# Kernel tuning notes

Measured on AMD Instinct MI355X. Metric: run time of the kernel, lower is better.

Reference implementation:

```python
import jax, jax.numpy as jnp
import numpy as np

B, T, I, H, O = 32, 2048, 12, 512, 3
L = 3  # GRU layers


def _gru_layer(x_seq, h0, w_ih, w_hh, b_ih, b_hh):
    # x_seq: [B,T,D], h0: [B,H]; PyTorch gate order: r, z, n
    xW = jnp.einsum('btd,gd->btg', x_seq, w_ih) + b_ih  # [B,T,3H]

    def step(h, xw_t):
        hw = h @ w_hh.T + b_hh                  # [B,3H]
        xr, xz, xn = jnp.split(xw_t, 3, axis=-1)
        hr, hz, hn = jnp.split(hw, 3, axis=-1)
        r = jax.nn.sigmoid(xr + hr)
        z = jax.nn.sigmoid(xz + hz)
        n = jnp.tanh(xn + r * hn)
        h_new = (1.0 - z) * n + z * h
        return h_new, h_new

    h_last, ys = jax.lax.scan(step, h0, jnp.swapaxes(xW, 0, 1))  # ys: [T,B,H]
    return jnp.swapaxes(ys, 0, 1), h_last


def _prelu(x, a):
    return jnp.where(x >= 0, x, a * x)


def setup_inputs() -> dict:
    key = jax.random.key(0)
    ks = jax.random.split(key, 40)
    s = 1.0 / np.sqrt(H)

    def u(k, shape):
        return jax.random.uniform(k, shape, jnp.float32, -s, s)

    inp = {
        'x': jax.random.normal(ks[0], (B, T, I), jnp.float32),
        'vel_init': jax.random.normal(ks[1], (B, 1, 3), jnp.float32),
    }
    in_dims = [I, H, H]
    for l in range(L):
        inp[f'w_ih_{l}'] = u(ks[2 + 4 * l], (3 * H, in_dims[l]))
        inp[f'w_hh_{l}'] = u(ks[3 + 4 * l], (3 * H, H))
        inp[f'b_ih_{l}'] = u(ks[4 + 4 * l], (3 * H,))
        inp[f'b_hh_{l}'] = u(ks[5 + 4 * l], (3 * H,))
    inp['a1'] = jnp.array([0.25], jnp.float32)  # PReLU (single shared param)
    inp['dec_in_w'] = u(ks[14], (H, I)); inp['dec_in_b'] = u(ks[15], (H,))
    inp['vd0_w'] = u(ks[16], (H, 3)); inp['vd0_b'] = u(ks[17], (H,))
    inp['vd1_w'] = u(ks[18], (H, 3)); inp['vd1_b'] = u(ks[19], (H,))
    inp['vd2_w'] = u(ks[20], (H, 3)); inp['vd2_b'] = u(ks[21], (H,))
    inp['vel_w'] = u(ks[22], (O, H)); inp['vel_b'] = u(ks[23], (O,))
    inp['std_w'] = u(ks[24], (O, H)); inp['std_b'] = u(ks[25], (O,))
    inp['attn_w'] = u(ks[26], (1, H)); inp['attn_b'] = u(ks[27], (1,))
    return inp


def reference(x, vel_init, w_ih_0, w_hh_0, b_ih_0, b_hh_0,
              w_ih_1, w_hh_1, b_ih_1, b_hh_1,
              w_ih_2, w_hh_2, b_ih_2, b_hh_2,
              a1, dec_in_w, dec_in_b,
              vd0_w, vd0_b, vd1_w, vd1_b, vd2_w, vd2_b,
              vel_w, vel_b, std_w, std_b, attn_w, attn_b):
    v0 = vel_init[:, 0, :]  # [B,3]
    # h0 per layer from velocity decoders (permute(1,0,2)+cat -> layer axis)
    h0s = [v0 @ vd0_w.T + vd0_b, v0 @ vd1_w.T + vd1_b, v0 @ vd2_w.T + vd2_b]
    w_ih = [w_ih_0, w_ih_1, w_ih_2]
    w_hh = [w_hh_0, w_hh_1, w_hh_2]
    b_ih = [b_ih_0, b_ih_1, b_ih_2]
    b_hh = [b_hh_0, b_hh_1, b_hh_2]

    out = x
    for l in range(L):
        out, _ = _gru_layer(out, h0s[l], w_ih[l], w_hh[l], b_ih[l], b_hh[l])

    out = _prelu(out, a1)
    # softmax skip-attention over time dim
    scores = jnp.einsum('bth,oh->bto', out, attn_w) + attn_b      # [B,T,1]
    attn = jax.nn.softmax(scores, axis=1)
    out = out + attn * (jnp.einsum('bti,hi->bth', x, dec_in_w) + dec_in_b)

    vel = jnp.einsum('bth,oh->bto', out, vel_w) + vel_b
    std = jnp.einsum('bth,oh->bto', out, std_w) + std_b
    return vel, std
```

## Files before the change

### kernel.cpp

```cpp
#include <hip/hip_runtime.h>
#include <stdint.h>


#define B_ 32
#define T_ 2048
#define H_ 512
#define R_ 128
#define HR_ 8

typedef __attribute__((ext_vector_type(8))) short s8v;
typedef __attribute__((ext_vector_type(4))) float f4v;
typedef __attribute__((ext_vector_type(4))) uint32_t u32x4;
typedef __attribute__((ext_vector_type(2))) unsigned short u16x2;

__device__ __forceinline__ uint16_t f2bf(float f){ return __builtin_bit_cast(uint16_t, (__bf16)f); }
__device__ __forceinline__ float bf2f(uint16_t b){ return __builtin_bit_cast(float, ((uint32_t)b)<<16); }

__device__ __forceinline__ s8v pack8(const float* f){
  s8v r;
  #pragma unroll
  for (int i=0;i<8;++i) r[i] = (short)f2bf(f[i]);
  return r;
}
__device__ __forceinline__ f4v mfma16(s8v a, s8v b, f4v c){
  return __builtin_amdgcn_mfma_f32_16x16x32_bf16(a,b,c,0,0,0);
}
#if __has_builtin(__builtin_amdgcn_rcpf)
__device__ __forceinline__ float rcp_(float x){ return __builtin_amdgcn_rcpf(x); }
#else
__device__ __forceinline__ float rcp_(float x){ return 1.0f/x; }
#endif
__device__ __forceinline__ float sigm(float s){ return rcp_(1.f + __expf(-s)); }
__device__ __forceinline__ float tanh2(float v){ return 1.f - 2.f*rcp_(1.f + __expf(2.f*v)); }

__device__ __forceinline__ u32x4 load_x4_sc(const void* p){
  u32x4 r;
  asm volatile("global_load_dwordx4 %0, %1, off sc0 sc1" : "=v"(r) : "v"(p) : "memory");
  return r;
}
__device__ __forceinline__ u32x4 load_x4_sc_wait(const void* p){
  u32x4 r;
  asm volatile("global_load_dwordx4 %0, %1, off sc0 sc1\n\ts_waitcnt vmcnt(0)"
               : "=v"(r) : "v"(p) : "memory");
  return r;
}
__device__ __forceinline__ uint32_t load_u32_sc_wait(const void* p){
  uint32_t r;
  asm volatile("global_load_dword %0, %1, off sc0 sc1\n\ts_waitcnt vmcnt(0)"
               : "=v"(r) : "v"(p) : "memory");
  return r;
}
__device__ __forceinline__ void store_s16_sc(void* p, uint32_t v){
  asm volatile("global_store_short %0, %1, off sc0 sc1" :: "v"(p), "v"(v) : "memory");
}
__device__ __forceinline__ void store_u32_sc(void* p, uint32_t v){
  asm volatile("global_store_dword %0, %1, off sc0 sc1" :: "v"(p), "v"(v) : "memory");
}
__device__ __forceinline__ u32x4 load_x4_l2(const void* p){
  u32x4 r;
  asm volatile("global_load_dwordx4 %0, %1, off sc0" : "=v"(r) : "v"(p) : "memory");
  return r;
}
__device__ __forceinline__ void store_s16_l2(void* p, uint32_t v){
  asm volatile("global_store_short %0, %1, off sc0" :: "v"(p), "v"(v) : "memory");
}

__device__ __forceinline__ void load16(u32x4* a, const uint16_t* base, bool l2){
  if (l2) {
    #pragma unroll
    for (int ks=0; ks<16; ++ks) a[ks] = load_x4_l2(base + ks*32);
  } else {
    #pragma unroll
    for (int ks=0; ks<16; ++ks) a[ks] = load_x4_sc(base + ks*32);
  }
}

__device__ __forceinline__ bool chunk_ok(u32x4 c){
  u16x2 m = __builtin_bit_cast(u16x2, c[0]);
  m = __builtin_elementwise_max(m, __builtin_bit_cast(u16x2, c[1]));
  m = __builtin_elementwise_max(m, __builtin_bit_cast(u16x2, c[2]));
  m = __builtin_elementwise_max(m, __builtin_bit_cast(u16x2, c[3]));
  unsigned short mm = (m[0] > m[1]) ? m[0] : m[1];
  return mm != (unsigned short)0xFFFFu;
}
__device__ __forceinline__ bool valid16(const u32x4* a){
  u16x2 m = {0, 0};
  #pragma unroll
  for (int c=0;c<16;++c){
    #pragma unroll
    for (int i=0;i<4;++i)
      m = __builtin_elementwise_max(m, __builtin_bit_cast(u16x2, a[c][i]));
  }
  unsigned short mm = (m[0] > m[1]) ? m[0] : m[1];
  return mm != (unsigned short)0xFFFFu;
}

__device__ __forceinline__ uint32_t get_xcc(){
  uint32_t x;
  asm volatile("s_getreg_b32 %0, hwreg(HW_REG_XCC_ID)" : "=s"(x));
  return x & 7u;
}
__device__ __forceinline__ uint64_t realtime_(){
  uint64_t t;
  asm volatile("s_memrealtime %0\n\ts_waitcnt lgkmcnt(0)" : "=s"(t));
  return t;
}

__global__ void poison_kernel(uint32_t* p, unsigned int n16)
{
  u32x4 v = {0xFFFFFFFFu, 0xFFFFFFFFu, 0xFFFFFFFFu, 0xFFFFFFFFu};
  for (unsigned int k = blockIdx.x*blockDim.x + threadIdx.x; k < n16;
       k += gridDim.x*blockDim.x)
    ((u32x4*)p)[k] = v;
}

__global__ void init_kernel(const float* __restrict__ vel_init,
    const float* __restrict__ w0, const float* __restrict__ b0,
    const float* __restrict__ w1, const float* __restrict__ b1,
    const float* __restrict__ w2, const float* __restrict__ b2,
    float* __restrict__ h0f, uint16_t* __restrict__ h0b,
    uint32_t* progress, uint32_t* claimp)
{
  const int l = blockIdx.x, tid = threadIdx.x;
  const float* w  = (l==0)?w0:((l==1)?w1:w2);
  const float* bb = (l==0)?b0:((l==1)?b1:b2);
  for (int idx = tid; idx < B_*H_; idx += 256){
    int b = idx >> 9, j = idx & 511;
    float s = bb[j] + vel_init[b*3+0]*w[j*3+0] + vel_init[b*3+1]*w[j*3+1]
                    + vel_init[b*3+2]*w[j*3+2];
    h0f[(size_t)l*(B_*H_) + idx] = s;
    h0b[(size_t)l*(B_*H_) + idx] = f2bf(s);
  }
  if (l == 0 && tid < 192) progress[tid] = 0;
  if (l == 0 && tid >= 192 && tid < 200) claimp[tid-192] = 0;
}

struct ScanParams {
  const float* x;
  const float* wih[3];
  const float* whh[3];
  const float* bih[3];
  const float* bhh[3];
  const float* h0f;
  const uint16_t* h0b;
  uint16_t* xr0;
  uint16_t* xr1;
  uint16_t* hr0;
  uint16_t* hr1;
  uint16_t* out2;
  uint32_t* progress;
  uint32_t* claimp;
};

__global__ __launch_bounds__(128, 1) void fused_scan(ScanParams P)
{
  const int tid  = threadIdx.x;
  const int lane = tid & 63;
  const int mt   = tid >> 6;
  const int u    = lane & 15;
  const int lq   = lane >> 4;
  const int ko   = lq * 8;
  const int bd   = lq * 4;

  __shared__ uint16_t lds[48*512];
  __shared__ char pad_[36864];
  __shared__ int sh_role[3];
  if (P.x == nullptr) ((volatile char*)pad_)[0] = 1;

  if (tid == 0){
    int layer = -1, wg = -1, home = 0;
    uint32_t xcc = get_xcc();
    if (xcc < 3u){
      unsigned s = atomicAdd(&P.claimp[xcc], 1u);
      if (s < 32u){ layer = (int)xcc; wg = (int)s; home = 1; }
    }
    if (layer < 0){
      uint64_t t0 = realtime_();
      while (realtime_() - t0 < 5000ull) __builtin_amdgcn_s_sleep(32);
      for (;;){
        bool allfull = true;
        for (int l=0; l<3 && layer<0; ++l){
          if (__hip_atomic_load(&P.claimp[l], __ATOMIC_RELAXED,
                                __HIP_MEMORY_SCOPE_AGENT) < 32u){
            allfull = false;
            unsigned s = atomicAdd(&P.claimp[l], 1u);
            if (s < 32u){ layer = l; wg = (int)s; home = (xcc == (uint32_t)l); }
          }
        }
        if (layer >= 0 || allfull) break;
        __builtin_amdgcn_s_sleep(16);
      }
    }
    int fast = 0;
    if (layer >= 0){
      if (!home) atomicAdd(&P.claimp[4], 1u);
      __hip_atomic_fetch_add(&P.claimp[3], 1u, __ATOMIC_ACQ_REL,
                             __HIP_MEMORY_SCOPE_AGENT);
      while (__hip_atomic_load(&P.claimp[3], __ATOMIC_ACQUIRE,
                               __HIP_MEMORY_SCOPE_AGENT) < 96u)
        __builtin_amdgcn_s_sleep(8);
      fast = (__hip_atomic_load(&P.claimp[4], __ATOMIC_ACQUIRE,
                                __HIP_MEMORY_SCOPE_AGENT) == 0u) ? 1 : 0;
    }
    sh_role[0] = layer; sh_role[1] = wg; sh_role[2] = fast;
  }
  __syncthreads();
  const int layer = sh_role[0];
  if (layer < 0) return;
  const int wg = sh_role[1];
  const bool fastmode = (sh_role[2] != 0);
  const int j0 = wg * 16;

  const float* wih = P.wih[layer];
  const float* whh = P.whh[layer];
  const float* bih = P.bih[layer];
  const float* bhh = P.bhh[layer];

  const float bs0 = bih[0*H_ + j0 + u] + bhh[0*H_ + j0 + u];
  const float bs1 = bih[1*H_ + j0 + u] + bhh[1*H_ + j0 + u];
  const float bi2 = bih[2*H_ + j0 + u];
  const float bh2 = bhh[2*H_ + j0 + u];

  s8v whhf[3][16];
  #pragma unroll
  for (int nt=0; nt<3; ++nt){
    #pragma unroll
    for (int ks=0; ks<16; ++ks){
      const float* wp = whh + (size_t)(nt*H_ + j0 + u)*H_ + ks*32 + ko;
      float tmp[8];
      #pragma unroll
      for (int i=0;i<8;++i) tmp[i] = wp[i];
      whhf[nt][ks] = pack8(tmp);
    }
  }

  s8v w0f[3];
  if (layer == 0){
    #pragma unroll
    for (int nt=0; nt<3; ++nt){
      float tmp[8];
      #pragma unroll
      for (int i=0;i<8;++i){
        int k = ko + i;
        tmp[i] = (k < 12) ? wih[(size_t)(nt*H_ + j0 + u)*12 + k] : 0.f;
      }
      w0f[nt] = pack8(tmp);
    }
  } else {
    for (int e = tid; e < (48*512)/8; e += 128) {
      int idx = e * 8;
      int g = idx >> 9, k = idx & 511;
      const float* wp = wih + (size_t)((g>>4)*H_ + j0 + (g&15))*H_ + k;
      float tmp[8];
      #pragma unroll
      for (int i=0;i<8;++i) tmp[i] = wp[i];
      s8v v = pack8(tmp);
      uint32_t msk = (uint32_t)((((g&7) ^ (((g>>3)&1)<<1))) << 4);
      uint32_t off = (uint32_t)g*1024u + ((((uint32_t)k)*2u) ^ msk);
      *(u32x4*)((char*)lds + off) = __builtin_bit_cast(u32x4, v);
    }
  }
  __syncthreads();

  const uint16_t* inring = (layer==1) ? P.xr0 : P.xr1;
  uint16_t* hring = (layer==0) ? P.hr0 : P.hr1;
  uint16_t* xout  = (layer==0) ? P.xr0 : P.xr1;
  uint32_t* myprog = P.progress + layer*64 + wg*2 + mt;
  const uint32_t* nextprog = (layer<2) ? (P.progress + (layer+1)*64) : nullptr;

  float hold[4];
  #pragma unroll
  for (int r=0;r<4;++r)
    hold[r] = P.h0f[(size_t)layer*(B_*H_) + (size_t)(mt*16 + bd + r)*H_ + j0 + u];

  const uint32_t sw  = (uint32_t)((((u&7) ^ (((u>>3)&1)<<1))) << 4);
  const uint32_t gb0 = (uint32_t)((0*16 + u) * 1024);
  const uint32_t gb1 = (uint32_t)((1*16 + u) * 1024);
  const uint32_t gb2 = (uint32_t)((2*16 + u) * 1024);
  const uint32_t koB = (uint32_t)(ko * 2);
  const int cl = lane & 31;
  const size_t rowoff = (size_t)(mt*16 + bd)*H_ + j0 + u;

  bool hfast = fastmode;
  int poison_until = 63;

  u32x4 xa[16];
  auto issue_x = [&](int tt){
    const uint16_t* xin = inring + (size_t)(tt & (R_-1))*(B_*H_)
                          + (size_t)(mt*16+u)*H_ + ko;
    #pragma unroll
    for (int ks=0; ks<16; ++ks) xa[ks] = load_x4_sc(xin + ks*32);
  };
  if (layer > 0) issue_x(0);

  for (int t = 0; t < T_; ++t) {
    f4v ac0 = {0,0,0,0}, ac1 = {0,0,0,0}, axn = {0,0,0,0}, ahn = {0,0,0,0};

    if (layer > 0) {
      asm volatile("s_waitcnt vmcnt(0)" ::: "memory");
      __builtin_amdgcn_sched_barrier(0);
      if (__ballot(valid16(xa)) != ~0ull) {
        const uint16_t* xslot = inring + (size_t)(t & (R_-1))*(B_*H_);
        const uint16_t* xcan  = xslot + (size_t)(mt*16)*H_ + cl*16;
        do {
          while (1) {
            u32x4 c = load_x4_sc_wait(xcan);
            if (__ballot(chunk_ok(c)) == ~0ull) break;
            __builtin_amdgcn_s_sleep(2);
          }
          issue_x(t);
          asm volatile("s_waitcnt vmcnt(0)" ::: "memory");
          __builtin_amdgcn_sched_barrier(0);
        } while (__ballot(valid16(xa)) != ~0ull);
      }
    }

    const uint16_t* hsrc = (t == 0)
        ? (P.h0b + (size_t)layer*(B_*H_))
        : (layer == 2 ? (P.out2 + (size_t)(t-1)*(B_*H_))
                      : (hring + (size_t)((t-1) & (HR_-1))*(B_*H_)));
    const uint16_t* hp = hsrc + (size_t)(mt*16+u)*H_ + ko;
    u32x4 ha[16];
    load16(ha, hp, hfast);

    if (layer == 0) {
      const float* xp = P.x + ((size_t)(mt*16 + u)*T_ + (size_t)t)*12;
      float4 lo  = *(const float4*)(xp);
      float4 md  = *(const float4*)(xp + 4);
      float4 hi4 = *(const float4*)(xp + 8);
      float xv[8];
      xv[0] = (ko==0) ? lo.x : hi4.x;  xv[1] = (ko==0) ? lo.y : hi4.y;
      xv[2] = (ko==0) ? lo.z : hi4.z;  xv[3] = (ko==0) ? lo.w : hi4.w;
      xv[4] = (ko==0) ? md.x : 0.f;    xv[5] = (ko==0) ? md.y : 0.f;
      xv[6] = (ko==0) ? md.z : 0.f;    xv[7] = (ko==0) ? md.w : 0.f;
      s8v a = pack8(xv);
      ac0 = mfma16(a, w0f[0], ac0);
      ac1 = mfma16(a, w0f[1], ac1);
      axn = mfma16(a, w0f[2], axn);
    } else {
      #pragma unroll
      for (int ks=0; ks<16; ++ks){
        s8v a = __builtin_bit_cast(s8v, xa[ks]);
        uint32_t kk = ((uint32_t)(ks*64) + koB) ^ sw;
        s8v w0 = *(const s8v*)((const char*)lds + gb0 + kk);
        s8v w1 = *(const s8v*)((const char*)lds + gb1 + kk);
        s8v w2 = *(const s8v*)((const char*)lds + gb2 + kk);
        ac0 = mfma16(a, w0, ac0);
        ac1 = mfma16(a, w1, ac1);
        axn = mfma16(a, w2, axn);
      }
    }

    asm volatile("s_waitcnt vmcnt(0)" ::: "memory");
    __builtin_amdgcn_sched_barrier(0);
    if (t > 0) {
      int spins = 0;
      while (__ballot(valid16(ha)) != ~0ull) {
        if (++spins > 512) hfast = false;
        __builtin_amdgcn_s_sleep(1);
        load16(ha, hp, hfast);
        asm volatile("s_waitcnt vmcnt(0)" ::: "memory");
        __builtin_amdgcn_sched_barrier(0);
      }
    }

    #pragma unroll
    for (int ks=0; ks<16; ++ks){
      s8v a = __builtin_bit_cast(s8v, ha[ks]);
      ac0 = mfma16(a, whhf[0][ks], ac0);
      ac1 = mfma16(a, whhf[1][ks], ac1);
      ahn = mfma16(a, whhf[2][ks], ahn);
    }

    if (layer < 2) {
      uint16_t* hrow = hring + (size_t)(t & (HR_-1))*(B_*H_) + rowoff;
      uint16_t* xrow = xout  + (size_t)(t & (R_-1))*(B_*H_) + rowoff;
      #pragma unroll
      for (int r=0;r<4;++r){
        float rg = sigm(ac0[r] + bs0);
        float zg = sigm(ac1[r] + bs1);
        float ng = tanh2(axn[r] + bi2 + rg*(ahn[r] + bh2));
        float hv = ng + zg*(hold[r] - ng);
        hold[r] = hv;
        uint32_t bv = (uint32_t)f2bf(hv);
        if (fastmode) store_s16_l2(hrow + (size_t)r*H_, bv);
        else          store_s16_sc(hrow + (size_t)r*H_, bv);
        store_s16_sc(xrow + (size_t)r*H_, bv);
      }
      uint16_t* prow = hring + (size_t)((t+4) & (HR_-1))*(B_*H_) + rowoff;
      #pragma unroll
      for (int r=0;r<4;++r){
        if (fastmode) store_s16_l2(prow + (size_t)r*H_, 0xFFFFu);
        else          store_s16_sc(prow + (size_t)r*H_, 0xFFFFu);
      }
    } else {
      uint16_t* orow = P.out2 + (size_t)t*(B_*H_) + rowoff;
      #pragma unroll
      for (int r=0;r<4;++r){
        float rg = sigm(ac0[r] + bs0);
        float zg = sigm(ac1[r] + bs1);
        float ng = tanh2(axn[r] + bi2 + rg*(ahn[r] + bh2));
        float hv = ng + zg*(hold[r] - ng);
        hold[r] = hv;
        uint32_t bv = (uint32_t)f2bf(hv);
        if (fastmode) store_s16_l2(orow + (size_t)r*H_, bv);
        else          store_s16_sc(orow + (size_t)r*H_, bv);
      }
    }

    if (layer > 0 && (t & 15) == 15 && lane == 0)
      store_u32_sc(myprog, (uint32_t)t);

    if (layer < 2 && t >= 64) {
      if (t > poison_until) {
        while (1) {
          int c = (int)load_u32_sc_wait(nextprog + lane);
          #pragma unroll
          for (int off=32; off>0; off>>=1){
            int c2 = __shfl_xor(c, off, 64);
            c = (c2 < c) ? c2 : c;
          }
          poison_until = c + 60;
          if (t <= poison_until) break;
          __builtin_amdgcn_s_sleep(8);
        }
      }
      uint16_t* qrow = xout + (size_t)((t+64) & (R_-1))*(B_*H_) + rowoff;
      #pragma unroll
      for (int r=0;r<4;++r) store_s16_sc(qrow + (size_t)r*H_, 0xFFFFu);
    }

    if (layer > 0 && t+1 < T_) issue_x(t+1);
  }
}

__global__ void scores_kernel(const uint16_t* __restrict__ out2,
    const float* __restrict__ attn_w, const float* __restrict__ attn_b,
    const float* __restrict__ a1, float* __restrict__ scores)
{
  int gw = (blockIdx.x * blockDim.x + threadIdx.x) >> 6;
  int lane = threadIdx.x & 63;
  int b = gw >> 11, t = gw & 2047;
  float alpha = a1[0];
  u32x4 q = *(const u32x4*)(out2 + ((size_t)t*B_ + b)*H_ + lane*8);
  const uint16_t* ob = (const uint16_t*)&q;
  const float* aw = attn_w + lane*8;
  float acc = 0.f;
  #pragma unroll
  for (int i=0;i<8;++i){
    float ov = bf2f(ob[i]);
    ov = (ov >= 0.f) ? ov : alpha*ov;
    acc += ov * aw[i];
  }
  #pragma unroll
  for (int off=32; off>0; off>>=1) acc += __shfl_xor(acc, off, 64);
  if (lane == 0) scores[(size_t)b*T_ + t] = acc + attn_b[0];
}

__global__ void softmax_kernel(const float* __restrict__ scores, float* __restrict__ attn)
{
  int b = blockIdx.x, tid = threadIdx.x;
  __shared__ float red[256];
  const float* row = scores + (size_t)b*T_;
  float v[8]; float m = -3.4e38f;
  #pragma unroll
  for (int i=0;i<8;++i){ v[i] = row[tid + i*256]; m = fmaxf(m, v[i]); }
  red[tid] = m; __syncthreads();
  for (int s=128; s>0; s>>=1){ if (tid < s) red[tid] = fmaxf(red[tid], red[tid+s]); __syncthreads(); }
  m = red[0]; __syncthreads();
  float sum = 0.f;
  #pragma unroll
  for (int i=0;i<8;++i){ v[i] = __expf(v[i]-m); sum += v[i]; }
  red[tid] = sum; __syncthreads();
  for (int s=128; s>0; s>>=1){ if (tid < s) red[tid] += red[tid+s]; __syncthreads(); }
  float inv = 1.f / red[0];
  #pragma unroll
  for (int i=0;i<8;++i) attn[(size_t)b*T_ + tid + i*256] = v[i]*inv;
}

__global__ void final_kernel(const uint16_t* __restrict__ out2, const float* __restrict__ x,
    const float* __restrict__ attn, const float* __restrict__ dw, const float* __restrict__ db,
    const float* __restrict__ vw, const float* __restrict__ vb,
    const float* __restrict__ swt, const float* __restrict__ sb,
    const float* __restrict__ a1, float* __restrict__ dout)
{
  int gw = (blockIdx.x * blockDim.x + threadIdx.x) >> 6;
  int lane = threadIdx.x & 63;
  int b = gw >> 11, t = gw & 2047;
  float alpha = a1[0];
  u32x4 q = *(const u32x4*)(out2 + ((size_t)t*B_ + b)*H_ + lane*8);
  const uint16_t* ob = (const uint16_t*)&q;
  const float* xp = x + ((size_t)b*T_ + t)*12;
  float xr[12];
  #pragma unroll
  for (int i=0;i<12;++i) xr[i] = xp[i];
  float av = attn[(size_t)b*T_ + t];
  float acc[6] = {0,0,0,0,0,0};
  #pragma unroll
  for (int k=0;k<8;++k){
    int j = lane*8 + k;
    float ov = bf2f(ob[k]);
    ov = (ov >= 0.f) ? ov : alpha*ov;
    float d = db[j];
    const float* dwp = dw + (size_t)j*12;
    #pragma unroll
    for (int i=0;i<12;++i) d += xr[i]*dwp[i];
    float uo = ov + av*d;
    #pragma unroll
    for (int o=0;o<3;++o){
      acc[o]   += uo * vw[(size_t)o*H_ + j];
      acc[3+o] += uo * swt[(size_t)o*H_ + j];
    }
  }
  #pragma unroll
  for (int o=0;o<6;++o){
    #pragma unroll
    for (int off=32; off>0; off>>=1) acc[o] += __shfl_xor(acc[o], off, 64);
  }
  if (lane == 0){
    size_t p = ((size_t)b*T_ + t)*3;
    #pragma unroll
    for (int o=0;o<3;++o){
      dout[p + o] = acc[o] + vb[o];
      dout[(size_t)B_*T_*3 + p + o] = acc[3+o] + sb[o];
    }
  }
}

extern "C" void kernel_launch(void* const* d_in, const int* in_sizes, int n_in,
                              void* d_out, int out_size, void* d_ws, size_t ws_size,
                              hipStream_t stream)
{
  (void)in_sizes; (void)n_in; (void)out_size; (void)ws_size;
  const float* x        = (const float*)d_in[0];
  const float* vel_init = (const float*)d_in[1];
  const float* w_ih[3] = {(const float*)d_in[2], (const float*)d_in[6],  (const float*)d_in[10]};
  const float* w_hh[3] = {(const float*)d_in[3], (const float*)d_in[7],  (const float*)d_in[11]};
  const float* b_ih[3] = {(const float*)d_in[4], (const float*)d_in[8],  (const float*)d_in[12]};
  const float* b_hh[3] = {(const float*)d_in[5], (const float*)d_in[9],  (const float*)d_in[13]};
  const float* a1     = (const float*)d_in[14];
  const float* dec_w  = (const float*)d_in[15];
  const float* dec_b  = (const float*)d_in[16];
  const float* vd_w[3] = {(const float*)d_in[17], (const float*)d_in[19], (const float*)d_in[21]};
  const float* vd_b[3] = {(const float*)d_in[18], (const float*)d_in[20], (const float*)d_in[22]};
  const float* vel_w  = (const float*)d_in[23];
  const float* vel_b  = (const float*)d_in[24];
  const float* std_w  = (const float*)d_in[25];
  const float* std_b  = (const float*)d_in[26];
  const float* attn_w = (const float*)d_in[27];
  const float* attn_b = (const float*)d_in[28];

  char* ws = (char*)d_ws;
  uint16_t* out2   = (uint16_t*)(ws);
  uint16_t* xr0    = (uint16_t*)(ws + (size_t)67108864);
  uint16_t* xr1    = (uint16_t*)(ws + (size_t)71303168);
  uint16_t* hr0    = (uint16_t*)(ws + (size_t)75497472);
  uint16_t* hr1    = (uint16_t*)(ws + (size_t)75759616);
  float*    h0f    = (float*)   (ws + (size_t)76021760);
  uint16_t* h0b    = (uint16_t*)(ws + (size_t)76218368);
  float*    scores = (float*)   (ws + (size_t)76316672);
  float*    attnp  = (float*)   (ws + (size_t)76578816);
  uint32_t* progress = (uint32_t*)(ws + (size_t)76840960);
  uint32_t* claimp   = (uint32_t*)(ws + (size_t)76841728);

  poison_kernel<<<2048, 256, 0, stream>>>((uint32_t*)ws, 76021760u/16u);
  init_kernel<<<3, 256, 0, stream>>>(vel_init, vd_w[0], vd_b[0], vd_w[1], vd_b[1],
                                     vd_w[2], vd_b[2], h0f, h0b, progress, claimp);

  ScanParams P;
  P.x = x;
  for (int l=0;l<3;++l){ P.wih[l]=w_ih[l]; P.whh[l]=w_hh[l]; P.bih[l]=b_ih[l]; P.bhh[l]=b_hh[l]; }
  P.h0f = h0f; P.h0b = h0b;
  P.xr0 = xr0; P.xr1 = xr1; P.hr0 = hr0; P.hr1 = hr1;
  P.out2 = out2; P.progress = progress; P.claimp = claimp;

  fused_scan<<<256, 128, 0, stream>>>(P);

  scores_kernel<<<(B_*T_)/4, 256, 0, stream>>>(out2, attn_w, attn_b, a1, scores);
  softmax_kernel<<<B_, 256, 0, stream>>>(scores, attnp);
  final_kernel<<<(B_*T_)/4, 256, 0, stream>>>(out2, x, attnp, dec_w, dec_b,
                                              vel_w, vel_b, std_w, std_b, a1, (float*)d_out);
}
```

Baseline: 8.520 ms.

## Replace poison-based x ring handoff with progress-counter sync between GRU layers

Layers now synchronise on the inter-layer x ring through per-workgroup progress counters instead of poisoning slots and spinning on sentinel values. Layer 2 gets its own small recurrent h ring rather than reading back from the large output buffer. The poison kernel now clears only the h rings, not the whole 76MB workspace. This removes the large poison launch and the ring-poison stores, and it overlaps the h load with waiting on x, at the cost of polling the counters and a vmcnt drain every 16 steps.

```diff
diff --git a/kernel.cpp b/kernel.cpp
--- a/kernel.cpp
+++ b/kernel.cpp
@@ -38,12 +38,6 @@
   asm volatile("global_load_dwordx4 %0, %1, off sc0 sc1" : "=v"(r) : "v"(p) : "memory");
   return r;
 }
-__device__ __forceinline__ u32x4 load_x4_sc_wait(const void* p){
-  u32x4 r;
-  asm volatile("global_load_dwordx4 %0, %1, off sc0 sc1\n\ts_waitcnt vmcnt(0)"
-               : "=v"(r) : "v"(p) : "memory");
-  return r;
-}
 __device__ __forceinline__ uint32_t load_u32_sc_wait(const void* p){
   uint32_t r;
   asm volatile("global_load_dword %0, %1, off sc0 sc1\n\ts_waitcnt vmcnt(0)"
@@ -65,8 +59,8 @@
   asm volatile("global_store_short %0, %1, off sc0" :: "v"(p), "v"(v) : "memory");
 }
 
-__device__ __forceinline__ void load16(u32x4* a, const uint16_t* base, bool l2){
-  if (l2) {
+__device__ __forceinline__ void load16f(u32x4* a, const uint16_t* base, bool fast){
+  if (fast) {
     #pragma unroll
     for (int ks=0; ks<16; ++ks) a[ks] = load_x4_l2(base + ks*32);
   } else {
@@ -74,15 +68,10 @@
     for (int ks=0; ks<16; ++ks) a[ks] = load_x4_sc(base + ks*32);
   }
 }
-
-__device__ __forceinline__ bool chunk_ok(u32x4 c){
-  u16x2 m = __builtin_bit_cast(u16x2, c[0]);
-  m = __builtin_elementwise_max(m, __builtin_bit_cast(u16x2, c[1]));
-  m = __builtin_elementwise_max(m, __builtin_bit_cast(u16x2, c[2]));
-  m = __builtin_elementwise_max(m, __builtin_bit_cast(u16x2, c[3]));
-  unsigned short mm = (m[0] > m[1]) ? m[0] : m[1];
-  return mm != (unsigned short)0xFFFFu;
-}
+__device__ __forceinline__ void st16f(void* p, uint32_t v, bool fast){
+  if (fast) store_s16_l2(p, v); else store_s16_sc(p, v);
+}
+
 __device__ __forceinline__ bool valid16(const u32x4* a){
   u16x2 m = {0, 0};
   #pragma unroll
@@ -147,6 +136,7 @@
   uint16_t* xr1;
   uint16_t* hr0;
   uint16_t* hr1;
+  uint16_t* hr2;
   uint16_t* out2;
   uint32_t* progress;
   uint32_t* claimp;
@@ -263,9 +253,10 @@
   __syncthreads();
 
   const uint16_t* inring = (layer==1) ? P.xr0 : P.xr1;
-  uint16_t* hring = (layer==0) ? P.hr0 : P.hr1;
-  uint16_t* xout  = (layer==0) ? P.xr0 : P.xr1;
+  uint16_t* xout = (layer==0) ? P.xr0 : P.xr1;
+  uint16_t* hring = (layer==0) ? P.hr0 : ((layer==1) ? P.hr1 : P.hr2);
   uint32_t* myprog = P.progress + layer*64 + wg*2 + mt;
+  const uint32_t* prevprog = (layer>0) ? (P.progress + (layer-1)*64) : nullptr;
   const uint32_t* nextprog = (layer<2) ? (P.progress + (layer+1)*64) : nullptr;
 
   float hold[4];
@@ -282,7 +273,9 @@
   const size_t rowoff = (size_t)(mt*16 + bd)*H_ + j0 + u;
 
   bool hfast = fastmode;
-  int poison_until = 63;
+  int xprog = 0;
+  int consprog = 0;
+  bool xpref = false;
 
   u32x4 xa[16];
   auto issue_x = [&](int tt){
@@ -291,37 +284,36 @@
     #pragma unroll
     for (int ks=0; ks<16; ++ks) xa[ks] = load_x4_sc(xin + ks*32);
   };
-  if (layer > 0) issue_x(0);
+  auto poll32 = [&](const uint32_t* base)->int{
+    int c = (int)load_u32_sc_wait(base + 2*cl + mt);
+    #pragma unroll
+    for (int off=16; off>0; off>>=1){
+      int c2 = __shfl_xor(c, off, 64);
+      c = (c2 < c) ? c2 : c;
+    }
+    return c;
+  };
 
   for (int t = 0; t < T_; ++t) {
     f4v ac0 = {0,0,0,0}, ac1 = {0,0,0,0}, axn = {0,0,0,0}, ahn = {0,0,0,0};
 
-    if (layer > 0) {
-      asm volatile("s_waitcnt vmcnt(0)" ::: "memory");
-      __builtin_amdgcn_sched_barrier(0);
-      if (__ballot(valid16(xa)) != ~0ull) {
-        const uint16_t* xslot = inring + (size_t)(t & (R_-1))*(B_*H_);
-        const uint16_t* xcan  = xslot + (size_t)(mt*16)*H_ + cl*16;
-        do {
-          while (1) {
-            u32x4 c = load_x4_sc_wait(xcan);
-            if (__ballot(chunk_ok(c)) == ~0ull) break;
-            __builtin_amdgcn_s_sleep(2);
-          }
-          issue_x(t);
-          asm volatile("s_waitcnt vmcnt(0)" ::: "memory");
-          __builtin_amdgcn_sched_barrier(0);
-        } while (__ballot(valid16(xa)) != ~0ull);
+    const uint16_t* hslot = (t == 0)
+        ? (P.h0b + (size_t)layer*(B_*H_))
+        : (hring + (size_t)((t-1) & (HR_-1))*(B_*H_));
+    const uint16_t* hp = hslot + (size_t)(mt*16+u)*H_ + ko;
+    u32x4 ha[16];
+    load16f(ha, hp, hfast);
+
+    if (layer > 0 && !xpref) {
+      while (xprog < t+1) {
+        xprog = poll32(prevprog);
+        if (xprog < t+1) __builtin_amdgcn_s_sleep(4);
       }
-    }
-
-    const uint16_t* hsrc = (t == 0)
-        ? (P.h0b + (size_t)layer*(B_*H_))
-        : (layer == 2 ? (P.out2 + (size_t)(t-1)*(B_*H_))
-                      : (hring + (size_t)((t-1) & (HR_-1))*(B_*H_)));
-    const uint16_t* hp = hsrc + (size_t)(mt*16+u)*H_ + ko;
-    u32x4 ha[16];
-    load16(ha, hp, hfast);
+      issue_x(t);
+    }
+
+    asm volatile("s_waitcnt vmcnt(0)" ::: "memory");
+    __builtin_amdgcn_sched_barrier(0);
 
     if (layer == 0) {
       const float* xp = P.x + ((size_t)(mt*16 + u)*T_ + (size_t)t)*12;
@@ -351,14 +343,12 @@
       }
     }
 
-    asm volatile("s_waitcnt vmcnt(0)" ::: "memory");
-    __builtin_amdgcn_sched_barrier(0);
     if (t > 0) {
       int spins = 0;
       while (__ballot(valid16(ha)) != ~0ull) {
         if (++spins > 512) hfast = false;
         __builtin_amdgcn_s_sleep(1);
-        load16(ha, hp, hfast);
+        load16f(ha, hp, hfast);
         asm volatile("s_waitcnt vmcnt(0)" ::: "memory");
         __builtin_amdgcn_sched_barrier(0);
       }
@@ -372,65 +362,46 @@
       ahn = mfma16(a, whhf[2][ks], ahn);
     }
 
-    if (layer < 2) {
-      uint16_t* hrow = hring + (size_t)(t & (HR_-1))*(B_*H_) + rowoff;
-      uint16_t* xrow = xout  + (size_t)(t & (R_-1))*(B_*H_) + rowoff;
-      #pragma unroll
-      for (int r=0;r<4;++r){
-        float rg = sigm(ac0[r] + bs0);
-        float zg = sigm(ac1[r] + bs1);
-        float ng = tanh2(axn[r] + bi2 + rg*(ahn[r] + bh2));
-        float hv = ng + zg*(hold[r] - ng);
-        hold[r] = hv;
-        uint32_t bv = (uint32_t)f2bf(hv);
-        if (fastmode) store_s16_l2(hrow + (size_t)r*H_, bv);
-        else          store_s16_sc(hrow + (size_t)r*H_, bv);
-        store_s16_sc(xrow + (size_t)r*H_, bv);
-      }
+    uint16_t* hrow = hring + (size_t)(t & (HR_-1))*(B_*H_) + rowoff;
+    uint16_t* xrow = (layer < 2)
+        ? (xout + (size_t)(t & (R_-1))*(B_*H_) + rowoff) : nullptr;
+    uint16_t* orow = (layer == 2)
+        ? (P.out2 + (size_t)t*(B_*H_) + rowoff) : nullptr;
+    #pragma unroll
+    for (int r=0;r<4;++r){
+      float rg = sigm(ac0[r] + bs0);
+      float zg = sigm(ac1[r] + bs1);
+      float ng = tanh2(axn[r] + bi2 + rg*(ahn[r] + bh2));
+      float hv = ng + zg*(hold[r] - ng);
+      hold[r] = hv;
+      uint32_t bv = (uint32_t)f2bf(hv);
+      st16f(hrow + (size_t)r*H_, bv, fastmode);
+      if (layer < 2) store_s16_sc(xrow + (size_t)r*H_, bv);
+      else           orow[(size_t)r*H_] = (uint16_t)bv;
+    }
+
+    {
       uint16_t* prow = hring + (size_t)((t+4) & (HR_-1))*(B_*H_) + rowoff;
       #pragma unroll
-      for (int r=0;r<4;++r){
-        if (fastmode) store_s16_l2(prow + (size_t)r*H_, 0xFFFFu);
-        else          store_s16_sc(prow + (size_t)r*H_, 0xFFFFu);
-      }
-    } else {
-      uint16_t* orow = P.out2 + (size_t)t*(B_*H_) + rowoff;
-      #pragma unroll
-      for (int r=0;r<4;++r){
-        float rg = sigm(ac0[r] + bs0);
-        float zg = sigm(ac1[r] + bs1);
-        float ng = tanh2(axn[r] + bi2 + rg*(ahn[r] + bh2));
-        float hv = ng + zg*(hold[r] - ng);
-        hold[r] = hv;
-        uint32_t bv = (uint32_t)f2bf(hv);
-        if (fastmode) store_s16_l2(orow + (size_t)r*H_, bv);
-        else          store_s16_sc(orow + (size_t)r*H_, bv);
-      }
-    }
-
-    if (layer > 0 && (t & 15) == 15 && lane == 0)
-      store_u32_sc(myprog, (uint32_t)t);
-
-    if (layer < 2 && t >= 64) {
-      if (t > poison_until) {
-        while (1) {
-          int c = (int)load_u32_sc_wait(nextprog + lane);
-          #pragma unroll
-          for (int off=32; off>0; off>>=1){
-            int c2 = __shfl_xor(c, off, 64);
-            c = (c2 < c) ? c2 : c;
-          }
-          poison_until = c + 60;
-          if (t <= poison_until) break;
-          __builtin_amdgcn_s_sleep(8);
-        }
-      }
-      uint16_t* qrow = xout + (size_t)((t+64) & (R_-1))*(B_*H_) + rowoff;
-      #pragma unroll
-      for (int r=0;r<4;++r) store_s16_sc(qrow + (size_t)r*H_, 0xFFFFu);
-    }
-
-    if (layer > 0 && t+1 < T_) issue_x(t+1);
+      for (int r=0;r<4;++r) st16f(prow + (size_t)r*H_, 0xFFFFu, fastmode);
+    }
+
+    if ((t & 15) == 15) {
+      asm volatile("s_waitcnt vmcnt(0)" ::: "memory");
+      if (lane == 0) store_u32_sc(myprog, (uint32_t)(t + 1));
+    }
+
+    if (layer < 2 && (t + 2 - R_) > consprog) {
+      do {
+        consprog = poll32(nextprog);
+        if (consprog < t + 2 - R_) __builtin_amdgcn_s_sleep(8);
+      } while (consprog < t + 2 - R_);
+    }
+
+    if (layer > 0) {
+      xpref = (t + 1 < T_) && (xprog >= t + 2);
+      if (xpref) issue_x(t + 1);
+    }
   }
 }
 
@@ -556,14 +527,15 @@
   uint16_t* xr1    = (uint16_t*)(ws + (size_t)71303168);
   uint16_t* hr0    = (uint16_t*)(ws + (size_t)75497472);
   uint16_t* hr1    = (uint16_t*)(ws + (size_t)75759616);
-  float*    h0f    = (float*)   (ws + (size_t)76021760);
-  uint16_t* h0b    = (uint16_t*)(ws + (size_t)76218368);
-  float*    scores = (float*)   (ws + (size_t)76316672);
-  float*    attnp  = (float*)   (ws + (size_t)76578816);
-  uint32_t* progress = (uint32_t*)(ws + (size_t)76840960);
-  uint32_t* claimp   = (uint32_t*)(ws + (size_t)76841728);
-
-  poison_kernel<<<2048, 256, 0, stream>>>((uint32_t*)ws, 76021760u/16u);
+  uint16_t* hr2    = (uint16_t*)(ws + (size_t)76021760);
+  float*    h0f    = (float*)   (ws + (size_t)76283904);
+  uint16_t* h0b    = (uint16_t*)(ws + (size_t)76480512);
+  float*    scores = (float*)   (ws + (size_t)76578816);
+  float*    attnp  = (float*)   (ws + (size_t)76840960);
+  uint32_t* progress = (uint32_t*)(ws + (size_t)77103104);
+  uint32_t* claimp   = (uint32_t*)(ws + (size_t)77103872);
+
+  poison_kernel<<<128, 256, 0, stream>>>((uint32_t*)hr0, 786432u/16u);
   init_kernel<<<3, 256, 0, stream>>>(vel_init, vd_w[0], vd_b[0], vd_w[1], vd_b[1],
                                      vd_w[2], vd_b[2], h0f, h0b, progress, claimp);
 
@@ -571,7 +543,7 @@
   P.x = x;
   for (int l=0;l<3;++l){ P.wih[l]=w_ih[l]; P.whh[l]=w_hh[l]; P.bih[l]=b_ih[l]; P.bhh[l]=b_hh[l]; }
   P.h0f = h0f; P.h0b = h0b;
-  P.xr0 = xr0; P.xr1 = xr1; P.hr0 = hr0; P.hr1 = hr1;
+  P.xr0 = xr0; P.xr1 = xr1; P.hr0 = hr0; P.hr1 = hr1; P.hr2 = hr2;
   P.out2 = out2; P.progress = progress; P.claimp = claimp;
 
   fused_scan<<<256, 128, 0, stream>>>(P);
```

After: 10.45 ms. 22.7% more time.
